# Optimization experiments

Hardware: AMD Instinct MI355X
Metric: run time of the kernel (lower is better)

The kernel has to match this reference:

```python
import jax, jax.numpy as jnp
import numpy as np

N_NODES = 100000
N_EDGES = 1600000
D_IN = 128
D_OUT = 128


def setup_inputs() -> dict:
    key = jax.random.key(0)
    k1, k2, k3, k4 = jax.random.split(key, 4)
    feat = jax.random.normal(k1, (N_NODES, D_IN), dtype=jnp.float32)
    # xavier_uniform on [D_IN, D_OUT]
    limit = float(np.sqrt(6.0 / (D_IN + D_OUT)))
    weight = jax.random.uniform(k2, (D_IN, D_OUT), minval=-limit, maxval=limit, dtype=jnp.float32)
    bias = jnp.zeros((D_OUT,), dtype=jnp.float32)
    src = jax.random.randint(k3, (N_EDGES,), 0, N_NODES, dtype=jnp.int32)
    dst = jax.random.randint(k4, (N_EDGES,), 0, N_NODES, dtype=jnp.int32)
    return {"feat": feat, "weight": weight, "bias": bias, "src": src, "dst": dst}


def reference(feat, weight, bias, src, dst):
    n = feat.shape[0]
    # in-degree of each node (number of incoming edges)
    deg = jax.ops.segment_sum(jnp.ones_like(dst, dtype=feat.dtype), dst, num_segments=n)
    norm = jnp.power(jnp.clip(deg, 1.0), -0.5)[:, None]  # [N, 1]
    # pre-normalize source features
    h = feat * norm
    # copy_src + sum aggregation: scatter-add messages from src to dst
    agg = jax.ops.segment_sum(h[src], dst, num_segments=n)  # [N, D_IN]
    # in_feats == out_feats -> matmul after aggregation (the else-branch)
    rst = jnp.matmul(agg, weight)
    rst = rst * norm + bias
    return rst
```

## Files before the change

kernel.cpp:

```cpp
#include <hip/hip_runtime.h>

#define D 128
#define BSHIFT 9
#define BNODES 512
#define BMASK 511
#define NB_MAX 256
#define STRIDE 10240
#define BIN_CHUNK 4096

typedef unsigned int uint;
typedef __attribute__((ext_vector_type(8))) short bf16x8;
typedef __attribute__((ext_vector_type(4))) float f32x4;

__device__ inline uint bf16_rne(float x) {
    uint u = __float_as_uint(x);
    return (u + 0x7fffu + ((u >> 16) & 1u)) >> 16;
}
__device__ inline uint pack2(float lo, float hi) {
    return bf16_rne(lo) | (bf16_rne(hi) << 16);
}

__global__ void __launch_bounds__(256) bin_kernel(const int* __restrict__ src,
                                                  const int* __restrict__ dst,
                                                  int* __restrict__ bucket_cur,
                                                  uint* __restrict__ binned,
                                                  int n_edges) {
    __shared__ int h[NB_MAX];
    __shared__ int base[NB_MAX];
    int t = threadIdx.x;
    long long e0 = (long long)blockIdx.x * BIN_CHUNK;
    h[t] = 0;
    __syncthreads();

    int d[16], s[16];
#pragma unroll
    for (int k = 0; k < 16; ++k) {
        long long idx = e0 + k * 256 + t;
        if (idx < n_edges) {
            d[k] = dst[idx];
            s[k] = src[idx];
            atomicAdd(&h[d[k] >> BSHIFT], 1);
        } else {
            d[k] = -1;
        }
    }
    __syncthreads();
    {
        int c = h[t];
        base[t] = c ? atomicAdd(&bucket_cur[t], c) : 0;
        h[t] = 0;
    }
    __syncthreads();
#pragma unroll
    for (int k = 0; k < 16; ++k) {
        if (d[k] >= 0) {
            int b = d[k] >> BSHIFT;
            int r = base[b] + atomicAdd(&h[b], 1);
            if (r < STRIDE)
                binned[(size_t)b * STRIDE + r] =
                    ((uint)s[k] << BSHIFT) | (uint)(d[k] & BMASK);
        }
    }
}

__global__ void __launch_bounds__(BNODES) fill2_kernel(
        const int* __restrict__ bucket_cur, uint* __restrict__ csr,
        float* __restrict__ norm, int* __restrict__ row_start,
        int* __restrict__ degp, int n_nodes) {
    __shared__ uint sbin[STRIDE];
    __shared__ int deg[BNODES];
    __shared__ int rs[BNODES];
    __shared__ int cur[BNODES];
    int b = blockIdx.x;
    int t = threadIdx.x;
    int cnt = bucket_cur[b];
    if (cnt > STRIDE) cnt = STRIDE;
    size_t gbase = (size_t)b * STRIDE;

    for (int k = t; k < cnt; k += BNODES) sbin[k] = csr[gbase + k];
    deg[t] = 0;
    __syncthreads();
    for (int k = t; k < cnt; k += BNODES) atomicAdd(&deg[sbin[k] & BMASK], 1);
    __syncthreads();

    int v = deg[t];
    rs[t] = v;
    __syncthreads();
    for (int o = 1; o < BNODES; o <<= 1) {
        int a = (t >= o) ? rs[t - o] : 0;
        __syncthreads();
        rs[t] += a;
        __syncthreads();
    }
    int excl = rs[t] - v;
    __syncthreads();
    rs[t] = excl;
    cur[t] = 0;

    int node = b * BNODES + t;
    if (node < n_nodes) {
        row_start[node] = (int)gbase + excl;
        degp[node] = v;
        norm[node] = rsqrtf(fmaxf((float)v, 1.0f));
    }
    __syncthreads();

    for (int k = t; k < cnt; k += BNODES) {
        uint p = sbin[k];
        int dl = p & BMASK;
        int r = atomicAdd(&cur[dl], 1);
        csr[gbase + rs[dl] + r] = p >> BSHIFT;
    }
}

__global__ void __launch_bounds__(256) prep_kernel(
        const float* __restrict__ feat, const float* __restrict__ norm,
        uint* __restrict__ h32, int n_nodes) {
    long long idx = (long long)blockIdx.x * 256 + threadIdx.x;
    if (idx >= (long long)n_nodes * 32) return;
    int i = (int)(idx >> 5);
    float nm = norm[i];
    float4 f = *(const float4*)(feat + idx * 4);
    uint2 o;
    o.x = pack2(f.x * nm, f.y * nm);
    o.y = pack2(f.z * nm, f.w * nm);
    *(uint2*)(h32 + idx * 2) = o;
}

__global__ void prep_w_kernel(const float* __restrict__ W,
                              uint4* __restrict__ wpack) {
    int idx = blockIdx.x * 256 + threadIdx.x;
    if (idx >= 2048) return;
    int lane = idx & 63;
    int ks = (idx >> 6) & 3;
    int ct = idx >> 8;
    int col = ct * 16 + (lane & 15);
    int k0 = ks * 32 + (lane >> 4) * 8;
    uint4 u;
    u.x = pack2(W[(k0 + 0) * D + col], W[(k0 + 1) * D + col]);
    u.y = pack2(W[(k0 + 2) * D + col], W[(k0 + 3) * D + col]);
    u.z = pack2(W[(k0 + 4) * D + col], W[(k0 + 5) * D + col]);
    u.w = pack2(W[(k0 + 6) * D + col], W[(k0 + 7) * D + col]);
    wpack[idx] = u;
}

#define UNPACK_ADD(u)                              \
    acc[0] += __uint_as_float((u).x << 16);        \
    acc[1] += __uint_as_float((u).x & 0xffff0000u);\
    acc[2] += __uint_as_float((u).y << 16);        \
    acc[3] += __uint_as_float((u).y & 0xffff0000u);\
    acc[4] += __uint_as_float((u).z << 16);        \
    acc[5] += __uint_as_float((u).z & 0xffff0000u);\
    acc[6] += __uint_as_float((u).w << 16);        \
    acc[7] += __uint_as_float((u).w & 0xffff0000u);

#define LDP 132

__global__ void __launch_bounds__(256) gather_mm_kernel(
        const uint4* __restrict__ h128, const uint* __restrict__ csr,
        const int* __restrict__ row_start, const int* __restrict__ degp,
        const float* __restrict__ norm, const uint4* __restrict__ wpack,
        const float* __restrict__ bias, float* __restrict__ out, int n) {
    __shared__ float As[16][LDP];
    int t = threadIdx.x;
    int lane = t & 63;
    int w = t >> 6;
    int r0 = blockIdx.x * 16;
    int g = lane >> 4;
    int c = lane & 15;

    for (int q = 0; q < 4; ++q) {
        int local = w * 4 + q;
        int i = r0 + local;
        float acc[8];
#pragma unroll
        for (int j = 0; j < 8; ++j) acc[j] = 0.f;

        if (i < n) {
            int beg = row_start[i];
            int end = beg + degp[i];
            for (int base = beg; base < end; base += 64) {
                int nk = end - base;
                if (nk > 64) nk = 64;
                int epre = (base + lane < end) ? (int)csr[base + lane] : 0;
                int k = 0;
                int kfull = nk & ~7;
                for (; k < kfull; k += 8) {
                    int s0 = __shfl(epre, k + g, 64);
                    int s1 = __shfl(epre, k + 4 + g, 64);
                    uint4 u0 = h128[(size_t)s0 * 16 + c];
                    uint4 u1 = h128[(size_t)s1 * 16 + c];
                    UNPACK_ADD(u0);
                    UNPACK_ADD(u1);
                }
                if (k < nk) {
                    int e0 = k + g;
                    int e1 = k + 4 + g;
                    int s0 = __shfl(epre, e0 & 63, 64);
                    int s1 = __shfl(epre, e1 & 63, 64);
                    uint4 z = {0u, 0u, 0u, 0u};
                    uint4 u0 = (e0 < nk) ? h128[(size_t)s0 * 16 + c] : z;
                    uint4 u1 = (e1 < nk) ? h128[(size_t)s1 * 16 + c] : z;
                    UNPACK_ADD(u0);
                    UNPACK_ADD(u1);
                }
            }
        }
#pragma unroll
        for (int j = 0; j < 8; ++j) {
            acc[j] += __shfl_xor(acc[j], 16, 64);
            acc[j] += __shfl_xor(acc[j], 32, 64);
        }
        if (g == 0) {
            float4 lo = {acc[0], acc[1], acc[2], acc[3]};
            float4 hi = {acc[4], acc[5], acc[6], acc[7]};
            *(float4*)&As[local][8 * c] = lo;
            *(float4*)&As[local][8 * c + 4] = hi;
        }
    }
    __syncthreads();

    uint4 afr[4];
#pragma unroll
    for (int ks = 0; ks < 4; ++ks) {
        const float* ap = &As[c][ks * 32 + g * 8];
        float4 f0 = *(const float4*)ap;
        float4 f1 = *(const float4*)(ap + 4);
        afr[ks].x = pack2(f0.x, f0.y);
        afr[ks].y = pack2(f0.z, f0.w);
        afr[ks].z = pack2(f1.x, f1.y);
        afr[ks].w = pack2(f1.z, f1.w);
    }

    float nm[4];
    int grow[4];
#pragma unroll
    for (int r = 0; r < 4; ++r) {
        grow[r] = r0 + g * 4 + r;
        int rc = grow[r] < n ? grow[r] : n - 1;
        nm[r] = norm[rc];
    }

#pragma unroll
    for (int cc = 0; cc < 2; ++cc) {
        int ct = 2 * w + cc;
        f32x4 acc = {0.f, 0.f, 0.f, 0.f};
#pragma unroll
        for (int ks = 0; ks < 4; ++ks) {
            uint4 bu = wpack[(ct * 4 + ks) * 64 + lane];
            acc = __builtin_amdgcn_mfma_f32_16x16x32_bf16(
                *(bf16x8*)&afr[ks], *(bf16x8*)&bu, acc, 0, 0, 0);
        }
        float bv = bias[ct * 16 + c];
#pragma unroll
        for (int r = 0; r < 4; ++r)
            if (grow[r] < n)
                out[(size_t)grow[r] * D + ct * 16 + c] = acc[r] * nm[r] + bv;
    }
}

extern "C" void kernel_launch(void* const* d_in, const int* in_sizes, int n_in,
                              void* d_out, int out_size, void* d_ws, size_t ws_size,
                              hipStream_t stream) {
    const float* feat   = (const float*)d_in[0];
    const float* weight = (const float*)d_in[1];
    const float* bias   = (const float*)d_in[2];
    const int*   src    = (const int*)d_in[3];
    const int*   dst    = (const int*)d_in[4];
    float* out = (float*)d_out;

    int n_nodes = in_sizes[0] / D;
    int n_edges = in_sizes[3];
    int nb = (n_nodes + BNODES - 1) >> BSHIFT;

    float* norm       = (float*)d_ws;
    int*   degp       = (int*)(norm + n_nodes);
    int*   row_start  = degp + n_nodes;
    int*   bucket_cur = row_start + n_nodes;
    uint*  csr        = (uint*)(bucket_cur + NB_MAX);
    uint*  h32        = csr + (size_t)nb * STRIDE;
    uint4* wpack      = (uint4*)(h32 + (size_t)n_nodes * 64);

    hipMemsetAsync(bucket_cur, 0, NB_MAX * sizeof(int), stream);

    bin_kernel<<<(n_edges + BIN_CHUNK - 1) / BIN_CHUNK, 256, 0, stream>>>(
        src, dst, bucket_cur, csr, n_edges);
    fill2_kernel<<<nb, BNODES, 0, stream>>>(bucket_cur, csr, norm, row_start,
                                            degp, n_nodes);
    prep_w_kernel<<<8, 256, 0, stream>>>(weight, wpack);
    prep_kernel<<<(n_nodes * 32 + 255) / 256, 256, 0, stream>>>(feat, norm, h32,
                                                                n_nodes);
    gather_mm_kernel<<<(n_nodes + 15) / 16, 256, 0, stream>>>(
        (const uint4*)h32, csr, row_start, degp, norm, wpack, bias, out, n_nodes);
}
```

Baseline: 132.8 us.

## Fuse weight packing and feature prep into binning/fill kernels with smaller buckets

Shrinks destination buckets from 512 to 128 nodes, giving about 782 fill blocks instead of about 196, so more of the GPU is busy. Weight packing moves into an extra block of the bin kernel, and the feature normalize-and-convert step moves into the fill kernel using per-bucket norms kept in shared memory. This removes two kernel launches and the separate norm reload, at the cost of longer fill blocks and a per-bucket capacity (STRIDE 2944) with less headroom against overflow.

Result: no change. 132.6 us (-0.1%).

```diff
diff --git a/kernel.cpp b/kernel.cpp
--- a/kernel.cpp
+++ b/kernel.cpp
@@ -1,11 +1,11 @@
 #include <hip/hip_runtime.h>
 
 #define D 128
-#define BSHIFT 9
-#define BNODES 512
-#define BMASK 511
-#define NB_MAX 256
-#define STRIDE 10240
+#define BSHIFT 7
+#define BNODES 128
+#define BMASK 127
+#define NB_MAX 1024
+#define STRIDE 2944
 #define BIN_CHUNK 4096
 
 typedef unsigned int uint;
@@ -24,12 +24,31 @@
                                                   const int* __restrict__ dst,
                                                   int* __restrict__ bucket_cur,
                                                   uint* __restrict__ binned,
-                                                  int n_edges) {
+                                                  const float* __restrict__ W,
+                                                  uint4* __restrict__ wpack,
+                                                  int n_edges, int nchunks) {
+    int t = threadIdx.x;
+    if (blockIdx.x == (uint)nchunks) {
+        for (int idx = t; idx < 2048; idx += 256) {
+            int lane = idx & 63;
+            int ks = (idx >> 6) & 3;
+            int ct = idx >> 8;
+            int col = ct * 16 + (lane & 15);
+            int k0 = ks * 32 + (lane >> 4) * 8;
+            uint4 u;
+            u.x = pack2(W[(k0 + 0) * D + col], W[(k0 + 1) * D + col]);
+            u.y = pack2(W[(k0 + 2) * D + col], W[(k0 + 3) * D + col]);
+            u.z = pack2(W[(k0 + 4) * D + col], W[(k0 + 5) * D + col]);
+            u.w = pack2(W[(k0 + 6) * D + col], W[(k0 + 7) * D + col]);
+            wpack[idx] = u;
+        }
+        return;
+    }
+
     __shared__ int h[NB_MAX];
     __shared__ int base[NB_MAX];
-    int t = threadIdx.x;
     long long e0 = (long long)blockIdx.x * BIN_CHUNK;
-    h[t] = 0;
+    for (int j = t; j < NB_MAX; j += 256) h[j] = 0;
     __syncthreads();
 
     int d[16], s[16];
@@ -45,10 +64,10 @@
         }
     }
     __syncthreads();
-    {
-        int c = h[t];
-        base[t] = c ? atomicAdd(&bucket_cur[t], c) : 0;
-        h[t] = 0;
+    for (int j = t; j < NB_MAX; j += 256) {
+        int c = h[j];
+        base[j] = c ? atomicAdd(&bucket_cur[j], c) : 0;
+        h[j] = 0;
     }
     __syncthreads();
 #pragma unroll
@@ -63,85 +82,77 @@
     }
 }
 
-__global__ void __launch_bounds__(BNODES) fill2_kernel(
+__global__ void __launch_bounds__(256) fill2_kernel(
         const int* __restrict__ bucket_cur, uint* __restrict__ csr,
-        float* __restrict__ norm, int* __restrict__ row_start,
-        int* __restrict__ degp, int n_nodes) {
+        const float* __restrict__ feat, float* __restrict__ norm,
+        int* __restrict__ row_start, int* __restrict__ degp,
+        uint* __restrict__ h32, int n_nodes) {
     __shared__ uint sbin[STRIDE];
     __shared__ int deg[BNODES];
     __shared__ int rs[BNODES];
     __shared__ int cur[BNODES];
+    __shared__ float snorm[BNODES];
     int b = blockIdx.x;
     int t = threadIdx.x;
     int cnt = bucket_cur[b];
     if (cnt > STRIDE) cnt = STRIDE;
     size_t gbase = (size_t)b * STRIDE;
 
-    for (int k = t; k < cnt; k += BNODES) sbin[k] = csr[gbase + k];
-    deg[t] = 0;
-    __syncthreads();
-    for (int k = t; k < cnt; k += BNODES) atomicAdd(&deg[sbin[k] & BMASK], 1);
-    __syncthreads();
-
-    int v = deg[t];
-    rs[t] = v;
+    for (int k = t; k < cnt; k += 256) sbin[k] = csr[gbase + k];
+    if (t < BNODES) deg[t] = 0;
+    __syncthreads();
+    for (int k = t; k < cnt; k += 256) atomicAdd(&deg[sbin[k] & BMASK], 1);
+    __syncthreads();
+
+    int v = 0;
+    if (t < BNODES) {
+        v = deg[t];
+        rs[t] = v;
+    }
     __syncthreads();
     for (int o = 1; o < BNODES; o <<= 1) {
-        int a = (t >= o) ? rs[t - o] : 0;
+        int a = (t < BNODES && t >= o) ? rs[t - o] : 0;
         __syncthreads();
-        rs[t] += a;
+        if (t < BNODES) rs[t] += a;
         __syncthreads();
     }
-    int excl = rs[t] - v;
-    __syncthreads();
-    rs[t] = excl;
-    cur[t] = 0;
-
-    int node = b * BNODES + t;
-    if (node < n_nodes) {
-        row_start[node] = (int)gbase + excl;
-        degp[node] = v;
-        norm[node] = rsqrtf(fmaxf((float)v, 1.0f));
-    }
-    __syncthreads();
-
-    for (int k = t; k < cnt; k += BNODES) {
+    if (t < BNODES) {
+        int excl = rs[t] - v;
+        rs[t] = excl;
+        cur[t] = 0;
+        int node = b * BNODES + t;
+        float nm = 0.f;
+        if (node < n_nodes) {
+            row_start[node] = (int)gbase + excl;
+            degp[node] = v;
+            nm = rsqrtf(fmaxf((float)v, 1.0f));
+            norm[node] = nm;
+        }
+        snorm[t] = nm;
+    }
+    __syncthreads();
+
+    for (int k = t; k < cnt; k += 256) {
         uint p = sbin[k];
         int dl = p & BMASK;
         int r = atomicAdd(&cur[dl], 1);
         csr[gbase + rs[dl] + r] = p >> BSHIFT;
     }
-}
-
-__global__ void __launch_bounds__(256) prep_kernel(
-        const float* __restrict__ feat, const float* __restrict__ norm,
-        uint* __restrict__ h32, int n_nodes) {
-    long long idx = (long long)blockIdx.x * 256 + threadIdx.x;
-    if (idx >= (long long)n_nodes * 32) return;
-    int i = (int)(idx >> 5);
-    float nm = norm[i];
-    float4 f = *(const float4*)(feat + idx * 4);
-    uint2 o;
-    o.x = pack2(f.x * nm, f.y * nm);
-    o.y = pack2(f.z * nm, f.w * nm);
-    *(uint2*)(h32 + idx * 2) = o;
-}
-
-__global__ void prep_w_kernel(const float* __restrict__ W,
-                              uint4* __restrict__ wpack) {
-    int idx = blockIdx.x * 256 + threadIdx.x;
-    if (idx >= 2048) return;
-    int lane = idx & 63;
-    int ks = (idx >> 6) & 3;
-    int ct = idx >> 8;
-    int col = ct * 16 + (lane & 15);
-    int k0 = ks * 32 + (lane >> 4) * 8;
-    uint4 u;
-    u.x = pack2(W[(k0 + 0) * D + col], W[(k0 + 1) * D + col]);
-    u.y = pack2(W[(k0 + 2) * D + col], W[(k0 + 3) * D + col]);
-    u.z = pack2(W[(k0 + 4) * D + col], W[(k0 + 5) * D + col]);
-    u.w = pack2(W[(k0 + 6) * D + col], W[(k0 + 7) * D + col]);
-    wpack[idx] = u;
+
+    int base_node = b * BNODES;
+    int rows = n_nodes - base_node;
+    if (rows > BNODES) rows = BNODES;
+    for (int u = t; u < rows * 32; u += 256) {
+        int row = u >> 5;
+        int part = u & 31;
+        int node = base_node + row;
+        float nm = snorm[row];
+        float4 f = *(const float4*)(feat + (size_t)node * D + part * 4);
+        uint2 o;
+        o.x = pack2(f.x * nm, f.y * nm);
+        o.y = pack2(f.z * nm, f.w * nm);
+        *(uint2*)(h32 + (size_t)node * 64 + part * 2) = o;
+    }
 }
 
 #define UNPACK_ADD(u)                              \
@@ -272,6 +283,7 @@
     int n_nodes = in_sizes[0] / D;
     int n_edges = in_sizes[3];
     int nb = (n_nodes + BNODES - 1) >> BSHIFT;
+    int nchunks = (n_edges + BIN_CHUNK - 1) / BIN_CHUNK;
 
     float* norm       = (float*)d_ws;
     int*   degp       = (int*)(norm + n_nodes);
@@ -283,13 +295,10 @@
 
     hipMemsetAsync(bucket_cur, 0, NB_MAX * sizeof(int), stream);
 
-    bin_kernel<<<(n_edges + BIN_CHUNK - 1) / BIN_CHUNK, 256, 0, stream>>>(
-        src, dst, bucket_cur, csr, n_edges);
-    fill2_kernel<<<nb, BNODES, 0, stream>>>(bucket_cur, csr, norm, row_start,
-                                            degp, n_nodes);
-    prep_w_kernel<<<8, 256, 0, stream>>>(weight, wpack);
-    prep_kernel<<<(n_nodes * 32 + 255) / 256, 256, 0, stream>>>(feat, norm, h32,
-                                                                n_nodes);
+    bin_kernel<<<nchunks + 1, 256, 0, stream>>>(src, dst, bucket_cur, csr,
+                                                weight, wpack, n_edges, nchunks);
+    fill2_kernel<<<nb, 256, 0, stream>>>(bucket_cur, csr, feat, norm, row_start,
+                                         degp, h32, n_nodes);
     gather_mm_kernel<<<(n_nodes + 15) / 16, 256, 0, stream>>>(
         (const uint4*)h32, csr, row_start, degp, norm, wpack, bias, out, n_nodes);
 }
```
